# Kernel tuning notes

Measured on AMD Instinct MI355X. Metric: run time of the kernel, lower is better.

Reference implementation:

```python
import jax, jax.numpy as jnp
import numpy as np


def setup_inputs() -> dict:
    key = jax.random.key(0)
    k1, k2, k3, k4, k5 = jax.random.split(key, 5)
    B, C, H, W = 32, 256, 64, 64
    R = 16  # reduction -> hidden = C // R = 16
    hid = C // R
    return {
        "x": jax.random.normal(k1, (B, C, H, W), dtype=jnp.float32),
        "w1": jax.random.normal(k2, (hid, 1, 1, 1), dtype=jnp.float32) * 0.1,
        "b1": jax.random.normal(k3, (hid,), dtype=jnp.float32) * 0.1,
        "w2": jax.random.normal(k4, (C, hid, 1, 1), dtype=jnp.float32) * 0.1,
        "b2": jax.random.normal(k5, (C,), dtype=jnp.float32) * 0.1,
    }


def reference(x, w1, b1, w2, b2):
    # PositionalAveragePooling: mean over channel dim -> [B, 1, H, W]
    s = jnp.mean(x, axis=1)  # [B, H, W]
    # conv1 (1 -> hid, 1x1): per-position scalar times weight vector + bias
    w1v = w1[:, 0, 0, 0]  # [hid]
    h = jax.nn.relu(s[:, None, :, :] * w1v[None, :, None, None]
                    + b1[None, :, None, None])  # [B, hid, H, W]
    # conv2 (hid -> C, 1x1): pointwise matmul over channel dim
    w2m = w2[:, :, 0, 0]  # [C, hid]
    scale = jax.nn.sigmoid(jnp.einsum("bkhw,ck->bchw", h, w2m)
                           + b2[None, :, None, None])  # [B, C, H, W]
    return x * scale
```

## Files before the change

kernel.cpp:

```cpp
#include <hip/hip_runtime.h>

#define NB 32
#define NC 256
#define NH 64
#define NW 64
#define NK 16
#define HW (NH * NW)

typedef float f32x4 __attribute__((ext_vector_type(4)));

__device__ __forceinline__ float fsig(float z) {
    return __builtin_amdgcn_rcpf(1.0f + __expf(-z));
}

__global__ __launch_bounds__(256, 4) void pse_kernel(
    const float* __restrict__ x,
    const float* __restrict__ w1,
    const float* __restrict__ b1,
    const float* __restrict__ w2,
    const float* __restrict__ b2,
    float* __restrict__ out)
{
    __shared__ float w2t[NK][NC + 4];
    __shared__ f32x4 part[16][17];
    __shared__ f32x4 hv4[NK][16];
    __shared__ f32x4 s4[16];
    __shared__ float b2s[NC];

    const int t  = threadIdx.x;
    const int cg = t >> 4;
    const int q  = t & 15;

    const int bh = blockIdx.x;
    const int b  = bh >> 6;
    const int h  = bh & 63;

    const size_t base = (size_t)b * NC * HW + (size_t)h * NW;
    const float* __restrict__ xp = x + base;
    float* __restrict__ op       = out + base;
    const float* __restrict__ xr = xp + (size_t)(cg << 4) * HW + (q << 2);

    f32x4 xv[16];
    #pragma unroll
    for (int i = 0; i < 16; ++i)
        xv[i] = __builtin_nontemporal_load(
            reinterpret_cast<const f32x4*>(xr + (size_t)i * HW));

    {
        const f32x4* __restrict__ w2v = reinterpret_cast<const f32x4*>(w2);
        #pragma unroll
        for (int r = 0; r < 4; ++r) {
            const int idx = t + (r << 8);
            const f32x4 v = w2v[idx];
            const int c  = idx >> 2;
            const int k0 = (idx & 3) << 2;
            w2t[k0 + 0][c] = v.x;
            w2t[k0 + 1][c] = v.y;
            w2t[k0 + 2][c] = v.z;
            w2t[k0 + 3][c] = v.w;
        }
        b2s[t] = b2[t];
    }

    {
        f32x4 p = (f32x4)(0.f);
        #pragma unroll
        for (int i = 0; i < 16; ++i) p += xv[i];
        part[cg][q] = p;
    }
    __syncthreads();

    if (t < 16) {
        f32x4 s = (f32x4)(0.f);
        #pragma unroll
        for (int i = 0; i < 16; ++i) s += part[i][t];
        s *= (1.0f / (float)NC);
        s4[t] = s;
    }
    __syncthreads();

    {
        const f32x4 s  = s4[q];
        const float w1k = w1[cg];
        const float b1k = b1[cg];
        f32x4 hvv;
        hvv.x = fmaxf(fmaf(s.x, w1k, b1k), 0.f);
        hvv.y = fmaxf(fmaf(s.y, w1k, b1k), 0.f);
        hvv.z = fmaxf(fmaf(s.z, w1k, b1k), 0.f);
        hvv.w = fmaxf(fmaf(s.w, w1k, b1k), 0.f);
        hv4[cg][q] = hvv;
    }
    __syncthreads();

    #pragma unroll
    for (int half = 0; half < 2; ++half) {
        const int c0 = (cg << 4) + (half << 3);

        f32x4 acc[8];
        #pragma unroll
        for (int j = 0; j < 8; ++j) acc[j] = (f32x4)(b2s[c0 + j]);

        #pragma unroll
        for (int k = 0; k < NK; ++k) {
            const f32x4 hk = hv4[k][q];
            const f32x4* __restrict__ wr =
                reinterpret_cast<const f32x4*>(&w2t[k][c0]);
            const f32x4 wa = wr[0], wb = wr[1];
            const float wv[8] = {wa.x, wa.y, wa.z, wa.w, wb.x, wb.y, wb.z, wb.w};
            #pragma unroll
            for (int j = 0; j < 8; ++j) {
                acc[j].x = fmaf(hk.x, wv[j], acc[j].x);
                acc[j].y = fmaf(hk.y, wv[j], acc[j].y);
                acc[j].z = fmaf(hk.z, wv[j], acc[j].z);
                acc[j].w = fmaf(hk.w, wv[j], acc[j].w);
            }
        }

        #pragma unroll
        for (int j = 0; j < 8; ++j) {
            const int i = (half << 3) + j;
            const f32x4 xvv = xv[i];
            f32x4 r;
            r.x = xvv.x * fsig(acc[j].x);
            r.y = xvv.y * fsig(acc[j].y);
            r.z = xvv.z * fsig(acc[j].z);
            r.w = xvv.w * fsig(acc[j].w);
            __builtin_nontemporal_store(r,
                reinterpret_cast<f32x4*>(op + (size_t)(c0 + j) * HW + (q << 2)));
        }
    }
}

extern "C" void kernel_launch(void* const* d_in, const int* in_sizes, int n_in,
                              void* d_out, int out_size, void* d_ws, size_t ws_size,
                              hipStream_t stream) {
    const float* x  = (const float*)d_in[0];
    const float* w1 = (const float*)d_in[1];
    const float* b1 = (const float*)d_in[2];
    const float* w2 = (const float*)d_in[3];
    const float* b2 = (const float*)d_in[4];
    float* out = (float*)d_out;

    dim3 grid(NB * NH);
    dim3 block(256);
    hipLaunchKernelGGL(pse_kernel, grid, block, 0, stream, x, w1, b1, w2, b2, out);
}
```

Measured before the change: 237.7 us.

## Use 1024-thread blocks with four channels per thread

Each block now has 1024 threads instead of 256, and each thread holds 4 channel rows instead of 16. The channel-mean reduction becomes a two-level shared-memory reduction, and the conv1 step is folded into that reduction phase. The goal is lower register pressure and more memory parallelism per CU. The cost is an extra barrier and the overhead of synchronizing larger blocks.

```diff
diff --git a/kernel.cpp b/kernel.cpp
--- a/kernel.cpp
+++ b/kernel.cpp
@@ -13,7 +13,7 @@
     return __builtin_amdgcn_rcpf(1.0f + __expf(-z));
 }
 
-__global__ __launch_bounds__(256, 4) void pse_kernel(
+__global__ __launch_bounds__(1024, 8) void pse_kernel(
     const float* __restrict__ x,
     const float* __restrict__ w1,
     const float* __restrict__ b1,
@@ -22,9 +22,9 @@
     float* __restrict__ out)
 {
     __shared__ float w2t[NK][NC + 4];
-    __shared__ f32x4 part[16][17];
+    __shared__ f32x4 part[64][17];
+    __shared__ f32x4 sA[16][17];
     __shared__ f32x4 hv4[NK][16];
-    __shared__ f32x4 s4[16];
     __shared__ float b2s[NC];
 
     const int t  = threadIdx.x;
@@ -38,96 +38,76 @@
     const size_t base = (size_t)b * NC * HW + (size_t)h * NW;
     const float* __restrict__ xp = x + base;
     float* __restrict__ op       = out + base;
-    const float* __restrict__ xr = xp + (size_t)(cg << 4) * HW + (q << 2);
+    const float* __restrict__ xr = xp + (size_t)(cg << 2) * HW + (q << 2);
 
-    f32x4 xv[16];
+    f32x4 xv[4];
     #pragma unroll
-    for (int i = 0; i < 16; ++i)
+    for (int i = 0; i < 4; ++i)
         xv[i] = __builtin_nontemporal_load(
             reinterpret_cast<const f32x4*>(xr + (size_t)i * HW));
 
     {
-        const f32x4* __restrict__ w2v = reinterpret_cast<const f32x4*>(w2);
-        #pragma unroll
-        for (int r = 0; r < 4; ++r) {
-            const int idx = t + (r << 8);
-            const f32x4 v = w2v[idx];
-            const int c  = idx >> 2;
-            const int k0 = (idx & 3) << 2;
-            w2t[k0 + 0][c] = v.x;
-            w2t[k0 + 1][c] = v.y;
-            w2t[k0 + 2][c] = v.z;
-            w2t[k0 + 3][c] = v.w;
-        }
-        b2s[t] = b2[t];
+        const f32x4 v = reinterpret_cast<const f32x4*>(w2)[t];
+        const int c  = t >> 2;
+        const int k0 = (t & 3) << 2;
+        w2t[k0 + 0][c] = v.x;
+        w2t[k0 + 1][c] = v.y;
+        w2t[k0 + 2][c] = v.z;
+        w2t[k0 + 3][c] = v.w;
+        if (t < NC) b2s[t] = b2[t];
     }
 
-    {
-        f32x4 p = (f32x4)(0.f);
-        #pragma unroll
-        for (int i = 0; i < 16; ++i) p += xv[i];
-        part[cg][q] = p;
+    part[cg][q] = xv[0] + xv[1] + xv[2] + xv[3];
+    __syncthreads();
+
+    if (t < 256) {
+        const int a = t >> 4;
+        sA[a][q] = part[4 * a + 0][q] + part[4 * a + 1][q]
+                 + part[4 * a + 2][q] + part[4 * a + 3][q];
     }
     __syncthreads();
 
-    if (t < 16) {
+    if (t < 256) {
+        const int k = t >> 4;
         f32x4 s = (f32x4)(0.f);
         #pragma unroll
-        for (int i = 0; i < 16; ++i) s += part[i][t];
+        for (int i = 0; i < 16; ++i) s += sA[i][q];
         s *= (1.0f / (float)NC);
-        s4[t] = s;
+        const float w1k = w1[k];
+        const float b1k = b1[k];
+        f32x4 hv;
+        hv.x = fmaxf(fmaf(s.x, w1k, b1k), 0.f);
+        hv.y = fmaxf(fmaf(s.y, w1k, b1k), 0.f);
+        hv.z = fmaxf(fmaf(s.z, w1k, b1k), 0.f);
+        hv.w = fmaxf(fmaf(s.w, w1k, b1k), 0.f);
+        hv4[k][q] = hv;
     }
     __syncthreads();
 
-    {
-        const f32x4 s  = s4[q];
-        const float w1k = w1[cg];
-        const float b1k = b1[cg];
-        f32x4 hvv;
-        hvv.x = fmaxf(fmaf(s.x, w1k, b1k), 0.f);
-        hvv.y = fmaxf(fmaf(s.y, w1k, b1k), 0.f);
-        hvv.z = fmaxf(fmaf(s.z, w1k, b1k), 0.f);
-        hvv.w = fmaxf(fmaf(s.w, w1k, b1k), 0.f);
-        hv4[cg][q] = hvv;
-    }
-    __syncthreads();
+    f32x4 acc[4];
+    #pragma unroll
+    for (int i = 0; i < 4; ++i) acc[i] = (f32x4)(b2s[(cg << 2) + i]);
 
     #pragma unroll
-    for (int half = 0; half < 2; ++half) {
-        const int c0 = (cg << 4) + (half << 3);
+    for (int k = 0; k < NK; ++k) {
+        const f32x4 hk = hv4[k][q];
+        const f32x4 wv = *reinterpret_cast<const f32x4*>(&w2t[k][cg << 2]);
+        acc[0] += hk * wv.x;
+        acc[1] += hk * wv.y;
+        acc[2] += hk * wv.z;
+        acc[3] += hk * wv.w;
+    }
 
-        f32x4 acc[8];
-        #pragma unroll
-        for (int j = 0; j < 8; ++j) acc[j] = (f32x4)(b2s[c0 + j]);
-
-        #pragma unroll
-        for (int k = 0; k < NK; ++k) {
-            const f32x4 hk = hv4[k][q];
-            const f32x4* __restrict__ wr =
-                reinterpret_cast<const f32x4*>(&w2t[k][c0]);
-            const f32x4 wa = wr[0], wb = wr[1];
-            const float wv[8] = {wa.x, wa.y, wa.z, wa.w, wb.x, wb.y, wb.z, wb.w};
-            #pragma unroll
-            for (int j = 0; j < 8; ++j) {
-                acc[j].x = fmaf(hk.x, wv[j], acc[j].x);
-                acc[j].y = fmaf(hk.y, wv[j], acc[j].y);
-                acc[j].z = fmaf(hk.z, wv[j], acc[j].z);
-                acc[j].w = fmaf(hk.w, wv[j], acc[j].w);
-            }
-        }
-
-        #pragma unroll
-        for (int j = 0; j < 8; ++j) {
-            const int i = (half << 3) + j;
-            const f32x4 xvv = xv[i];
-            f32x4 r;
-            r.x = xvv.x * fsig(acc[j].x);
-            r.y = xvv.y * fsig(acc[j].y);
-            r.z = xvv.z * fsig(acc[j].z);
-            r.w = xvv.w * fsig(acc[j].w);
-            __builtin_nontemporal_store(r,
-                reinterpret_cast<f32x4*>(op + (size_t)(c0 + j) * HW + (q << 2)));
-        }
+    #pragma unroll
+    for (int i = 0; i < 4; ++i) {
+        const f32x4 xvv = xv[i];
+        f32x4 r;
+        r.x = xvv.x * fsig(acc[i].x);
+        r.y = xvv.y * fsig(acc[i].y);
+        r.z = xvv.z * fsig(acc[i].z);
+        r.w = xvv.w * fsig(acc[i].w);
+        __builtin_nontemporal_store(r,
+            reinterpret_cast<f32x4*>(op + (size_t)((cg << 2) + i) * HW + (q << 2)));
     }
 }
 
@@ -142,6 +122,6 @@
     float* out = (float*)d_out;
 
     dim3 grid(NB * NH);
-    dim3 block(256);
+    dim3 block(1024);
     hipLaunchKernelGGL(pse_kernel, grid, block, 0, stream, x, w1, b1, w2, b2, out);
 }
```

Measured after the change: 228.8 us. 1.04x faster.
